# Optimization experiments

Measured on AMD Instinct MI355X. Metric: run time of the kernel, lower is better.

The kernel has to match this reference:

```python
import jax, jax.numpy as jnp
import numpy as np

N_ROI = 1024
N_CLASS = 21      # num_classes + 1
APP_DIM = 1024
D_F = 128
N_REL = 16
DIM_K = 64
DIM_G = 64


def loc2bbox(src, loc):
    # src, loc: [M,4] with (y0,x0,y1,x1) / (dy,dx,dh,dw)
    h = src[:, 2] - src[:, 0]
    w = src[:, 3] - src[:, 1]
    cy = src[:, 0] + 0.5 * h
    cx = src[:, 1] + 0.5 * w
    ncy = loc[:, 0] * h + cy
    ncx = loc[:, 1] * w + cx
    nh = jnp.exp(loc[:, 2]) * h
    nw = jnp.exp(loc[:, 3]) * w
    return jnp.stack([ncy - 0.5 * nh, ncx - 0.5 * nw,
                      ncy + 0.5 * nh, ncx + 0.5 * nw], axis=1)


def rank_embedding(n, feat_dim, wave_len=1000.0):
    rank = jnp.arange(n, dtype=jnp.float32)[:, None]
    fr = jnp.arange(feat_dim // 2, dtype=jnp.float32)
    dim_mat = 1.0 / (wave_len ** (fr / (feat_dim / 2.0)))
    mul = rank * dim_mat[None, :]
    return jnp.concatenate([jnp.sin(mul), jnp.cos(mul)], axis=-1)  # [n, feat_dim]


def positional_embedding(f_g, dim_g, wave_len=1000.0):
    # f_g: [N,4]; replicates the repo's PositionalEmbedding exactly
    x_min, y_min, x_max, y_max = jnp.split(f_g, 4, axis=1)  # [N,1] each
    cx = (x_min + x_max) * 0.5
    cy = (y_min + y_max) * 0.5
    w = (x_max - x_min) + 1.0
    h = (y_max - y_min) + 1.0
    dx = jnp.log(jnp.maximum(jnp.abs((cx - cx.T) / w), 1e-3))
    dy = jnp.log(jnp.maximum(jnp.abs((cy - cy.T) / h), 1e-3))
    dw = jnp.log(w / w.T)
    dh = jnp.log(h / h.T)
    pos = jnp.stack([dx, dy, dw, dh], axis=-1)               # [N,N,4]
    fr = jnp.arange(dim_g // 8, dtype=jnp.float32)
    dim_mat = 1.0 / (wave_len ** (fr / (dim_g / 8.0)))       # [dim_g/8]
    mul = (100.0 * pos)[..., None] * dim_mat                 # [N,N,4,dim_g/8]
    mul = mul.reshape(pos.shape[0], pos.shape[1], -1)
    return jnp.concatenate([jnp.sin(mul), jnp.cos(mul)], axis=-1)  # [N,N,dim_g]


def setup_inputs():
    key = jax.random.key(0)
    ks = jax.random.split(key, 16)
    yx = jax.random.uniform(ks[0], (N_ROI, 2), minval=0.0, maxval=500.0)
    hw = jax.random.uniform(ks[1], (N_ROI, 2), minval=16.0, maxval=128.0)
    sample_roi = jnp.concatenate([yx, yx + hw], axis=1)      # valid (y0,x0,y1,x1)
    roi_cls_loc = jax.random.normal(ks[2], (N_ROI, N_CLASS * 4)) * 0.5
    roi_score = jax.random.normal(ks[3], (N_ROI, N_CLASS))
    # force no background argmax -> nonzero() filter keeps all N (static shapes)
    roi_score = roi_score.at[:, 0].add(-10.0)
    appearance_features = jax.random.normal(ks[4], (N_ROI, APP_DIM))
    size = jnp.array([600, 800], dtype=jnp.int32)
    s = 0.02
    rank_w = jax.random.normal(ks[5], (APP_DIM, D_F)) * s
    rank_b = jnp.zeros((D_F,), jnp.float32)
    feat_w = jax.random.normal(ks[6], (APP_DIM, D_F)) * s
    feat_b = jnp.zeros((D_F,), jnp.float32)
    logit_w = jax.random.normal(ks[7], (APP_DIM, 1)) * s
    logit_b = jnp.zeros((1,), jnp.float32)
    wg_w = jax.random.normal(ks[8], (N_REL, DIM_G)) * s
    wg_b = jnp.full((N_REL,), 0.1, jnp.float32)  # keep some geo weights > 0
    wk_w = jax.random.normal(ks[9], (N_REL, D_F, DIM_K)) * s
    wk_b = jnp.zeros((N_REL, DIM_K), jnp.float32)
    wq_w = jax.random.normal(ks[10], (N_REL, D_F, DIM_K)) * s
    wq_b = jnp.zeros((N_REL, DIM_K), jnp.float32)
    wv_w = jax.random.normal(ks[11], (N_REL, D_F, DIM_K)) * s
    wv_b = jnp.zeros((N_REL, DIM_K), jnp.float32)
    return {"sample_roi": sample_roi, "roi_cls_loc": roi_cls_loc,
            "roi_score": roi_score, "appearance_features": appearance_features,
            "size": size,
            "rank_w": rank_w, "rank_b": rank_b, "feat_w": feat_w, "feat_b": feat_b,
            "logit_w": logit_w, "logit_b": logit_b,
            "wg_w": wg_w, "wg_b": wg_b, "wk_w": wk_w, "wk_b": wk_b,
            "wq_w": wq_w, "wq_b": wq_b, "wv_w": wv_w, "wv_b": wv_b}


def reference(sample_roi, roi_cls_loc, roi_score, appearance_features, size,
              rank_w, rank_b, feat_w, feat_b, logit_w, logit_b,
              wg_w, wg_b, wk_w, wk_b, wq_w, wq_b, wv_w, wv_b):
    n = sample_roi.shape[0]
    size_f = size.astype(jnp.float32)
    # loc denormalization (mean = 0)
    std = jnp.tile(jnp.array([0.1, 0.1, 0.2, 0.2], jnp.float32), N_CLASS)
    loc = (roi_cls_loc * std).reshape(-1, 4)                  # [N*21,4]
    roi_rep = jnp.broadcast_to(sample_roi[:, None, :], (n, N_CLASS, 4)).reshape(-1, 4)
    cls_bbox = loc2bbox(roi_rep, loc).reshape(n, N_CLASS, 4)
    # replicates original's clamp on class-strided slices of the [N,21,4] view
    cls_bbox = cls_bbox.at[:, 0::2].set(jnp.clip(cls_bbox[:, 0::2], 0.0, size_f[0]))
    cls_bbox = cls_bbox.at[:, 1::2].set(jnp.clip(cls_bbox[:, 1::2], 0.0, size_f[1]))
    prob_all = jax.nn.softmax(roi_score, axis=1)
    prob = jnp.max(prob_all, axis=-1)
    prob_argmax = jnp.argmax(prob_all, axis=-1)
    cls_bbox = cls_bbox[jnp.arange(n), prob_argmax]           # [N,4]
    # background filter; inputs guarantee all foreground -> static size n
    nz = jnp.nonzero(prob_argmax, size=n, fill_value=0)[0]
    prob_argmax = prob_argmax[nz]
    prob = prob[nz]
    cls_bbox = cls_bbox[nz]
    feats = appearance_features[nz]
    order = jnp.argsort(-prob)                                # descending
    sorted_prob = prob[order]
    sorted_cls_bboxes = cls_bbox[order]
    sorted_labels = prob_argmax[order]
    sorted_features = feats[order]
    nms_rank = rank_embedding(n, APP_DIM) @ rank_w + rank_b   # [N,D_F]
    emb_feat = sorted_features @ feat_w + feat_b + nms_rank   # [N,D_F]
    pos_emb = positional_embedding(sorted_cls_bboxes, DIM_G)  # [N,N,DIM_G]
    # 16 independent RelationUnits, batched as heads h
    w_g = jax.nn.relu(jnp.einsum('mng,hg->hmn', pos_emb, wg_w) + wg_b[:, None, None])
    k = jnp.einsum('nd,hdk->hnk', emb_feat, wk_w) + wk_b[:, None, :]
    q = jnp.einsum('nd,hdk->hnk', emb_feat, wq_w) + wq_b[:, None, :]
    v = jnp.einsum('nd,hdk->hnk', emb_feat, wv_w) + wv_b[:, None, :]
    # scaled_dot[m,n] = k_m . q_n (row m is 'key', softmax over n) per original
    scores = jnp.einsum('hmk,hnk->hmn', k, q) / np.sqrt(DIM_K).astype(np.float32)
    w_mn = jax.nn.softmax(jnp.log(jnp.maximum(w_g, 1e-6)) + scores, axis=-1)
    rel = jnp.einsum('hmn,hnk->hmk', w_mn, v)                 # [H,N,K]
    rel = rel.transpose(1, 0, 2).reshape(n, N_REL * DIM_K) + sorted_features
    s1 = jax.nn.sigmoid(rel @ logit_w + logit_b).reshape(-1)
    nms_scores = s1 * sorted_prob
    return nms_scores, sorted_labels - 1, sorted_cls_bboxes
```

## Files before the change

kernel.cpp:

```cpp
#include <hip/hip_runtime.h>
#include <hip/hip_bf16.h>
#include <math.h>

typedef unsigned long long u64;
typedef unsigned int u32;
typedef __hip_bfloat16 bf16;

#define N 1024
#define NCLS 21
#define APP 1024
#define DF 128
#define NH 16
#define DK 64
#define NS 4

typedef __attribute__((ext_vector_type(8))) short short8v;
typedef __attribute__((ext_vector_type(4))) float float4v;
union U4S8 { uint4 u; short8v s; };

__device__ __forceinline__ float b2f(bf16 x) { return __bfloat162float(x); }
__device__ __forceinline__ ushort f2bu(float x) { bf16 b = __float2bfloat16(x); return *(ushort*)&b; }

__global__ void k_prep(const float* __restrict__ roi, const float* __restrict__ cls_loc,
                       const float* __restrict__ score, const int* __restrict__ size,
                       float* __restrict__ prob, int* __restrict__ label,
                       float* __restrict__ bbox, u64* __restrict__ keys)
{
    int i = blockIdx.x * 256 + threadIdx.x;
    if (i >= N) return;
    float s[NCLS];
    float mx = -1e30f; int am = 0;
    for (int c = 0; c < NCLS; c++) {
        s[c] = score[i * NCLS + c];
        if (s[c] > mx) { mx = s[c]; am = c; }
    }
    float sum = 0.f;
    for (int c = 0; c < NCLS; c++) sum += expf(s[c] - mx);
    float p = 1.0f / sum;

    float y0 = roi[i*4+0], x0 = roi[i*4+1];
    float y1 = roi[i*4+2], x1 = roi[i*4+3];
    float hh = y1 - y0, ww = x1 - x0;
    float cy = y0 + 0.5f * hh, cx = x0 + 0.5f * ww;
    float l0 = cls_loc[i*84 + am*4 + 0] * 0.1f;
    float l1 = cls_loc[i*84 + am*4 + 1] * 0.1f;
    float l2 = cls_loc[i*84 + am*4 + 2] * 0.2f;
    float l3 = cls_loc[i*84 + am*4 + 3] * 0.2f;
    float ncy = l0 * hh + cy, ncx = l1 * ww + cx;
    float nh = expf(l2) * hh, nw = expf(l3) * ww;
    float b0 = ncy - 0.5f * nh, b1 = ncx - 0.5f * nw;
    float b2v = ncy + 0.5f * nh, b3 = ncx + 0.5f * nw;
    float lim = ((am & 1) == 0) ? (float)size[0] : (float)size[1];
    b0  = fminf(fmaxf(b0, 0.f), lim);
    b1  = fminf(fmaxf(b1, 0.f), lim);
    b2v = fminf(fmaxf(b2v, 0.f), lim);
    b3  = fminf(fmaxf(b3, 0.f), lim);
    prob[i] = p; label[i] = am;
    bbox[i*4+0] = b0; bbox[i*4+1] = b1; bbox[i*4+2] = b2v; bbox[i*4+3] = b3;
    keys[i] = ((u64)(0xFFFFFFFFu - __float_as_uint(p)) << 32) | (u32)i;
}

__global__ void __launch_bounds__(256) k_rank(
        const u64* __restrict__ keys, const float* __restrict__ prob,
        const int* __restrict__ label, const float* __restrict__ bbox,
        int* __restrict__ order, float* __restrict__ sprob,
        float* __restrict__ sbbox, float* __restrict__ out)
{
    __shared__ u64 sk[N];
    int t = threadIdx.x;
    int i = blockIdx.x * 256 + t;
    for (int j = t; j < N; j += 256) sk[j] = keys[j];
    __syncthreads();
    u64 my = sk[i];
    int r = 0;
    for (int j = 0; j < N; j++) r += (sk[j] < my) ? 1 : 0;
    order[r] = i;
    sprob[r] = prob[i];
    float b0 = bbox[i*4+0], b1 = bbox[i*4+1], b2 = bbox[i*4+2], b3 = bbox[i*4+3];
    sbbox[r*4+0] = b0; sbbox[r*4+1] = b1; sbbox[r*4+2] = b2; sbbox[r*4+3] = b3;
    out[N + r] = (float)(label[i] - 1);
    out[2*N + r*4 + 0] = b0;
    out[2*N + r*4 + 1] = b1;
    out[2*N + r*4 + 2] = b2;
    out[2*N + r*4 + 3] = b3;
}

__global__ void __launch_bounds__(256) k_emb3(
        const int* __restrict__ order, const float* __restrict__ app,
        const float* __restrict__ feat_w, const float* __restrict__ rank_w,
        float* __restrict__ part)
{
    __shared__ ushort sA[64][72];
    __shared__ ushort sW[128][72];
    __shared__ int sOrd[64];
    int rt = blockIdx.x, dc = blockIdx.y, ph = blockIdx.z, t = threadIdx.x;
    int r0 = rt * 64, d0 = dc * 64;
    int w = t >> 6, l = t & 63, l15 = l & 15, quad = l >> 4;
    if (t < 64) sOrd[t] = order[r0 + t];
    __syncthreads();

    const float* Wsrc = ph ? rank_w : feat_w;
    #pragma unroll
    for (int it = 0; it < 32; it++) {
        int idx = t + it * 256;
        int d = idx >> 7, c = idx & 127;
        sW[c][d] = f2bu(Wsrc[(size_t)(d0 + d) * 128 + c]);
    }
    if (ph == 0) {
        #pragma unroll
        for (int it = 0; it < 16; it++) {
            int idx = t + it * 256;
            int r = idx >> 6, d = idx & 63;
            sA[r][d] = f2bu(app[(size_t)sOrd[r] * 1024 + d0 + d]);
        }
    } else {
        #pragma unroll
        for (int it = 0; it < 16; it++) {
            int idx = t + it * 256;
            int r = idx >> 6, d = idx & 63;
            int dgl = d0 + d;
            float irow = (float)(r0 + r);
            float val;
            if (dgl < 512) val = __sinf(irow * exp2f(-(float)dgl * 0.019464422f));
            else           val = __cosf(irow * exp2f(-(float)(dgl - 512) * 0.019464422f));
            sA[r][d] = f2bu(val);
        }
    }
    __syncthreads();

    U4S8 Af0, Af1;
    Af0.u = *(uint4*)&sA[w*16 + l15][quad*8];
    Af1.u = *(uint4*)&sA[w*16 + l15][32 + quad*8];
    float4v acc[8];
    #pragma unroll
    for (int nb = 0; nb < 8; nb++) acc[nb] = (float4v){0.f, 0.f, 0.f, 0.f};
    #pragma unroll
    for (int nb = 0; nb < 8; nb++) {
        U4S8 Bf0, Bf1;
        Bf0.u = *(uint4*)&sW[nb*16 + l15][quad*8];
        Bf1.u = *(uint4*)&sW[nb*16 + l15][32 + quad*8];
        acc[nb] = __builtin_amdgcn_mfma_f32_16x16x32_bf16(Af0.s, Bf0.s, acc[nb], 0, 0, 0);
        acc[nb] = __builtin_amdgcn_mfma_f32_16x16x32_bf16(Af1.s, Bf1.s, acc[nb], 0, 0, 0);
    }
    #pragma unroll
    for (int reg = 0; reg < 4; reg++) {
        int row = r0 + w*16 + quad*4 + reg;
        #pragma unroll
        for (int nb = 0; nb < 8; nb++)
            part[(((size_t)ph * 16 + dc) * 1024 + row) * 128 + nb*16 + l15] = acc[nb][reg];
    }
}

__global__ void k_embsum(const float* __restrict__ part,
                         const float* __restrict__ feat_b, const float* __restrict__ rank_b,
                         bf16* __restrict__ embb)
{
    int gid = blockIdx.x * 256 + threadIdx.x;
    int c = gid & 127;
    float acc = feat_b[c] + rank_b[c];
    for (int dc = 0; dc < 32; dc++) acc += part[(size_t)dc * 131072 + gid];
    embb[gid] = __float2bfloat16(acc);
}

__global__ void __launch_bounds__(256) k_qkv2(
        const bf16* __restrict__ embb,
        const float* __restrict__ wq, const float* __restrict__ bq,
        const float* __restrict__ wk, const float* __restrict__ bk,
        const float* __restrict__ wv, const float* __restrict__ bv,
        bf16* __restrict__ q, bf16* __restrict__ k, bf16* __restrict__ v)
{
    __shared__ ushort sWt[64][136];
    int t = threadIdx.x;
    int rt = blockIdx.x, h = blockIdx.y, mat = blockIdx.z;
    const float* W  = (mat == 0) ? wq : (mat == 1) ? wk : wv;
    const float* Bb = (mat == 0) ? bq : (mat == 1) ? bk : bv;
    bf16* Out       = (mat == 0) ? q  : (mat == 1) ? k  : v;

    #pragma unroll
    for (int i = 0; i < 32; i++) {
        int idx = t + i * 256;
        int d = idx >> 6, kk = idx & 63;
        sWt[kk][d] = f2bu(W[((size_t)h * 128 + d) * 64 + kk]);
    }
    int w = t >> 6, l = t & 63, l15 = l & 15, quad = l >> 4;
    float biasv[4];
    #pragma unroll
    for (int nb = 0; nb < 4; nb++) biasv[nb] = Bb[h * 64 + nb*16 + l15];
    __syncthreads();

    U4S8 Bf[4][4];
    #pragma unroll
    for (int nb = 0; nb < 4; nb++)
        #pragma unroll
        for (int kc = 0; kc < 4; kc++)
            Bf[nb][kc].u = *(uint4*)&sWt[nb*16 + l15][kc*32 + quad*8];

    const uint4* A4 = (const uint4*)embb;
    int r0 = rt * 128 + w * 32;
    ushort* outu = (ushort*)Out;
    for (int mb = 0; mb < 2; mb++) {
        int arow = r0 + mb*16 + l15;
        U4S8 Af[4];
        #pragma unroll
        for (int kc = 0; kc < 4; kc++) Af[kc].u = A4[(size_t)arow * 16 + kc*4 + quad];
        float4v acc[4];
        #pragma unroll
        for (int nb = 0; nb < 4; nb++) acc[nb] = (float4v){0.f, 0.f, 0.f, 0.f};
        #pragma unroll
        for (int kc = 0; kc < 4; kc++)
            #pragma unroll
            for (int nb = 0; nb < 4; nb++)
                acc[nb] = __builtin_amdgcn_mfma_f32_16x16x32_bf16(Af[kc].s, Bf[nb][kc].s, acc[nb], 0, 0, 0);
        #pragma unroll
        for (int reg = 0; reg < 4; reg++) {
            int orow = r0 + mb*16 + quad*4 + reg;
            #pragma unroll
            for (int nb = 0; nb < 4; nb++)
                outu[((size_t)h * N + orow) * 64 + nb*16 + l15] = f2bu(acc[nb][reg] + biasv[nb]);
        }
    }
}

__global__ void __launch_bounds__(256) k_geo2(
        const float* __restrict__ sbbox, const float* __restrict__ wgw,
        const float* __restrict__ wgb, bf16* __restrict__ lw)
{
    __shared__ ushort sE[256][72];
    __shared__ uint   sOut[NH][132];
    __shared__ float  mbb[4];
    int m = blockIdx.x, nc = blockIdx.y, t = threadIdx.x;
    int w = t >> 6, l = t & 63, l15 = l & 15, quad = l >> 4;

    if (t == 0) {
        float b0 = sbbox[m*4+0], b1 = sbbox[m*4+1], b2 = sbbox[m*4+2], b3 = sbbox[m*4+3];
        mbb[0] = (b0 + b2) * 0.5f; mbb[1] = (b1 + b3) * 0.5f;
        mbb[2] = b2 - b0 + 1.0f;   mbb[3] = b3 - b1 + 1.0f;
    }
    U4S8 Bg0, Bg1;
    #pragma unroll
    for (int j = 0; j < 8; j++) {
        ((ushort*)&Bg0)[j] = f2bu(wgw[l15*64 + quad*8 + j]);
        ((ushort*)&Bg1)[j] = f2bu(wgw[l15*64 + 32 + quad*8 + j]);
    }
    float bias = wgb[l15];
    __syncthreads();

    int n = nc * 256 + t;
    float b0 = sbbox[n*4+0], b1 = sbbox[n*4+1], b2 = sbbox[n*4+2], b3 = sbbox[n*4+3];
    float cxn = (b0 + b2) * 0.5f, cyn = (b1 + b3) * 0.5f;
    float wn = b2 - b0 + 1.0f, hn = b3 - b1 + 1.0f;
    float dx = __logf(fmaxf(fabsf((mbb[0] - cxn) / mbb[2]), 1e-3f));
    float dy = __logf(fmaxf(fabsf((mbb[1] - cyn) / mbb[3]), 1e-3f));
    float dw = __logf(mbb[2] / wn);
    float dh = __logf(mbb[3] / hn);
    float pos[4] = { dx, dy, dw, dh };
    const float dmt[8] = { 1.0f, 0.42169650342f, 0.177827941f, 0.0749894209f,
                           0.0316227766f, 0.01333521432f, 0.00562341325f, 0.00237137371f };
    float args[32];
    #pragma unroll
    for (int c = 0; c < 4; c++)
        #pragma unroll
        for (int f = 0; f < 8; f++) args[c*8 + f] = 100.0f * pos[c] * dmt[f];
    uint* rowp = (uint*)&sE[t][0];
    #pragma unroll
    for (int jj = 0; jj < 16; jj++) {
        float s0 = __sinf(args[2*jj]), s1 = __sinf(args[2*jj+1]);
        rowp[jj] = (uint)f2bu(s0) | ((uint)f2bu(s1) << 16);
    }
    #pragma unroll
    for (int jj = 0; jj < 16; jj++) {
        float c0 = __cosf(args[2*jj]), c1 = __cosf(args[2*jj+1]);
        rowp[16 + jj] = (uint)f2bu(c0) | ((uint)f2bu(c1) << 16);
    }
    __syncthreads();

    #pragma unroll
    for (int mt2 = 0; mt2 < 4; mt2++) {
        int prow = w*64 + mt2*16 + l15;
        U4S8 Af0, Af1;
        Af0.u = *(uint4*)&sE[prow][quad*8];
        Af1.u = *(uint4*)&sE[prow][32 + quad*8];
        float4v c = (float4v){0.f, 0.f, 0.f, 0.f};
        c = __builtin_amdgcn_mfma_f32_16x16x32_bf16(Af0.s, Bg0.s, c, 0, 0, 0);
        c = __builtin_amdgcn_mfma_f32_16x16x32_bf16(Af1.s, Bg1.s, c, 0, 0, 0);
        float v0 = __logf(fmaxf(fmaxf(c[0] + bias, 0.f), 1e-6f));
        float v1 = __logf(fmaxf(fmaxf(c[1] + bias, 0.f), 1e-6f));
        float v2 = __logf(fmaxf(fmaxf(c[2] + bias, 0.f), 1e-6f));
        float v3 = __logf(fmaxf(fmaxf(c[3] + bias, 0.f), 1e-6f));
        int pb = (w*64 + mt2*16 + quad*4) >> 1;
        sOut[l15][pb]     = (uint)f2bu(v0) | ((uint)f2bu(v1) << 16);
        sOut[l15][pb + 1] = (uint)f2bu(v2) | ((uint)f2bu(v3) << 16);
    }
    __syncthreads();
    uint* lwu = (uint*)lw;
    #pragma unroll
    for (int it = 0; it < 8; it++) {
        int idx = t + it * 256;
        int hh = idx >> 7, col = idx & 127;
        lwu[((size_t)hh << 19) + ((size_t)m << 9) + nc*128 + col] = sOut[hh][col];
    }
}

__global__ void __launch_bounds__(256) k_attn4(
        const bf16* __restrict__ q, const bf16* __restrict__ kmat,
        const bf16* __restrict__ v, const bf16* __restrict__ lw,
        float* __restrict__ opart, float* __restrict__ mpart, float* __restrict__ zpart)
{
    __shared__ uint sQu[64][36];
    __shared__ uint sVtu[64][36];
    __shared__ uint slwu[64][36];
    __shared__ uint sPu[4][16][36];

    int t = threadIdx.x;
    int mt = blockIdx.x, h = blockIdx.y, ns = blockIdx.z;
    int m0 = mt * 64;
    int w = t >> 6, l = t & 63, l15 = l & 15, quad = l >> 4;

    U4S8 kf0, kf1;
    {
        const uint4* k4 = (const uint4*)kmat;
        size_t krow = ((size_t)h * N + m0 + w*16 + l15) * 8;
        kf0.u = k4[krow + quad];
        kf1.u = k4[krow + 4 + quad];
    }

    float4v O[4];
    float M[4], Z[4];
    #pragma unroll
    for (int i = 0; i < 4; i++) {
        O[i] = (float4v){0.f, 0.f, 0.f, 0.f};
        M[i] = -1e30f; Z[i] = 0.f;
    }

    const uint* qsrc = (const uint*)q;
    const uint* vsrc = (const uint*)v;
    const uint* lwsrc = (const uint*)lw;

    for (int tile = ns * (16/NS); tile < (ns + 1) * (16/NS); tile++) {
        int n0 = tile * 64;
        #pragma unroll
        for (int i = 0; i < 8; i++) {
            int idx = t + i * 256;
            int nj = idx >> 5, kp = idx & 31;
            sQu[nj][kp] = qsrc[((size_t)h * N + n0 + nj) * 32 + kp];
        }
        #pragma unroll
        for (int i = 0; i < 4; i++) {
            int idx = t + i * 256;
            int a = idx & 31, nh2 = idx >> 5;
            uint g0 = vsrc[((size_t)h * N + n0 + 2*nh2) * 32 + a];
            uint g1 = vsrc[((size_t)h * N + n0 + 2*nh2 + 1) * 32 + a];
            sVtu[2*a][nh2]     = (g0 & 0xFFFFu) | (g1 << 16);
            sVtu[2*a + 1][nh2] = (g0 >> 16) | (g1 & 0xFFFF0000u);
        }
        #pragma unroll
        for (int i = 0; i < 8; i++) {
            int idx = t + i * 256;
            int mi = idx >> 5, np = idx & 31;
            slwu[mi][np] = lwsrc[((size_t)h << 19) + ((size_t)(m0 + mi) << 9) + (n0 >> 1) + np];
        }
        __syncthreads();

        float4v S[4];
        #pragma unroll
        for (int nb = 0; nb < 4; nb++) {
            U4S8 bq0, bq1;
            bq0.u = *(uint4*)&sQu[nb*16 + l15][quad*4];
            bq1.u = *(uint4*)&sQu[nb*16 + l15][16 + quad*4];
            float4v zz = (float4v){0.f, 0.f, 0.f, 0.f};
            float4v p0 = __builtin_amdgcn_mfma_f32_16x16x32_bf16(kf0.s, bq0.s, zz, 0, 0, 0);
            S[nb] = __builtin_amdgcn_mfma_f32_16x16x32_bf16(kf1.s, bq1.s, p0, 0, 0, 0);
        }
        ushort* pRow[4];
        #pragma unroll
        for (int r = 0; r < 4; r++) pRow[r] = (ushort*)&sPu[w][quad*4 + r][0];
        #pragma unroll
        for (int r = 0; r < 4; r++) {
            int mi = w*16 + quad*4 + r;
            float sv[4];
            #pragma unroll
            for (int nb = 0; nb < 4; nb++) {
                int col = nb*16 + l15;
                uint lu = slwu[mi][col >> 1];
                float lv = (col & 1) ? __uint_as_float(lu & 0xFFFF0000u)
                                     : __uint_as_float(lu << 16);
                sv[nb] = S[nb][r] * 0.125f + lv;
            }
            float rm = fmaxf(fmaxf(sv[0], sv[1]), fmaxf(sv[2], sv[3]));
            #pragma unroll
            for (int off = 1; off < 16; off <<= 1)
                rm = fmaxf(rm, __shfl_xor(rm, off, 64));
            float newM = fmaxf(M[r], rm);
            float pr[4], rs = 0.f;
            #pragma unroll
            for (int nb = 0; nb < 4; nb++) {
                pr[nb] = __expf(sv[nb] - newM);
                rs += pr[nb];
            }
            #pragma unroll
            for (int off = 1; off < 16; off <<= 1)
                rs += __shfl_xor(rs, off, 64);
            float sc = __expf(M[r] - newM);
            M[r] = newM;
            Z[r] = Z[r] * sc + rs;
            #pragma unroll
            for (int kvb = 0; kvb < 4; kvb++) O[kvb][r] *= sc;
            #pragma unroll
            for (int nb = 0; nb < 4; nb++)
                pRow[r][nb*16 + l15] = f2bu(pr[nb]);
        }
        {
            U4S8 ap0, ap1;
            ap0.u = *(uint4*)&sPu[w][l15][quad*4];
            ap1.u = *(uint4*)&sPu[w][l15][16 + quad*4];
            #pragma unroll
            for (int kvb = 0; kvb < 4; kvb++) {
                U4S8 bv0, bv1;
                bv0.u = *(uint4*)&sVtu[kvb*16 + l15][quad*4];
                bv1.u = *(uint4*)&sVtu[kvb*16 + l15][16 + quad*4];
                O[kvb] = __builtin_amdgcn_mfma_f32_16x16x32_bf16(ap0.s, bv0.s, O[kvb], 0, 0, 0);
                O[kvb] = __builtin_amdgcn_mfma_f32_16x16x32_bf16(ap1.s, bv1.s, O[kvb], 0, 0, 0);
            }
        }
        __syncthreads();
    }

    #pragma unroll
    for (int r = 0; r < 4; r++) {
        int m = m0 + w*16 + quad*4 + r;
        size_t row = ((size_t)ns * NH + h) * N + m;
        #pragma unroll
        for (int kvb = 0; kvb < 4; kvb++)
            opart[row * 64 + kvb*16 + l15] = O[kvb][r];
        if (l15 == 0) { mpart[row] = M[r]; zpart[row] = Z[r]; }
    }
}

__global__ void __launch_bounds__(256) k_amerge(
        const float* __restrict__ opart, const float* __restrict__ mpart,
        const float* __restrict__ zpart, bf16* __restrict__ rel)
{
    int gid = blockIdx.x * 256 + threadIdx.x;
    int row = gid >> 4;
    int colq = gid & 15;
    float Ms[NS];
    float Mg = -1e30f;
    #pragma unroll
    for (int ns = 0; ns < NS; ns++) {
        Ms[ns] = mpart[(size_t)ns * 16384 + row];
        Mg = fmaxf(Mg, Ms[ns]);
    }
    float Zt = 0.f;
    float acc0 = 0.f, acc1 = 0.f, acc2 = 0.f, acc3 = 0.f;
    #pragma unroll
    for (int ns = 0; ns < NS; ns++) {
        float wgt = __expf(Ms[ns] - Mg);
        Zt += zpart[(size_t)ns * 16384 + row] * wgt;
        float4 o = *(const float4*)&opart[((size_t)ns * 16384 + row) * 64 + colq*4];
        acc0 += o.x * wgt; acc1 += o.y * wgt; acc2 += o.z * wgt; acc3 += o.w * wgt;
    }
    float inv = 1.0f / Zt;
    ushort* relu = (ushort*)rel;
    size_t base = (size_t)row * 64 + colq*4;
    relu[base + 0] = f2bu(acc0 * inv);
    relu[base + 1] = f2bu(acc1 * inv);
    relu[base + 2] = f2bu(acc2 * inv);
    relu[base + 3] = f2bu(acc3 * inv);
}

__global__ void k_final(const bf16* __restrict__ rel, const int* __restrict__ order,
                        const float* __restrict__ app, const float* __restrict__ lw,
                        const float* __restrict__ lb, const float* __restrict__ sprob,
                        float* __restrict__ out)
{
    __shared__ float red[2];
    int m = blockIdx.x, t = threadIdx.x;
    int o = order[m];
    float s = 0.f;
    for (int j = t; j < APP; j += 128) {
        int hh = j >> 6, kk = j & 63;
        float rv = b2f(rel[((size_t)hh * N + m) * DK + kk]) + app[o * APP + j];
        s += rv * lw[j];
    }
    #pragma unroll
    for (int off = 32; off > 0; off >>= 1) s += __shfl_down(s, off, 64);
    if ((t & 63) == 0) red[t >> 6] = s;
    __syncthreads();
    if (t == 0) {
        float tot = red[0] + red[1] + lb[0];
        float s1 = 1.0f / (1.0f + expf(-tot));
        out[m] = s1 * sprob[m];
    }
}

extern "C" void kernel_launch(void* const* d_in, const int* in_sizes, int n_in,
                              void* d_out, int out_size, void* d_ws, size_t ws_size,
                              hipStream_t stream)
{
    const float* roi      = (const float*)d_in[0];
    const float* cls_loc  = (const float*)d_in[1];
    const float* score    = (const float*)d_in[2];
    const float* app      = (const float*)d_in[3];
    const int*   size     = (const int*)d_in[4];
    const float* rank_w   = (const float*)d_in[5];
    const float* rank_b   = (const float*)d_in[6];
    const float* feat_w   = (const float*)d_in[7];
    const float* feat_b   = (const float*)d_in[8];
    const float* logit_w  = (const float*)d_in[9];
    const float* logit_b  = (const float*)d_in[10];
    const float* wg_w     = (const float*)d_in[11];
    const float* wg_b     = (const float*)d_in[12];
    const float* wk_w     = (const float*)d_in[13];
    const float* wk_b     = (const float*)d_in[14];
    const float* wq_w     = (const float*)d_in[15];
    const float* wq_b     = (const float*)d_in[16];
    const float* wv_w     = (const float*)d_in[17];
    const float* wv_b     = (const float*)d_in[18];
    float* out = (float*)d_out;

    char* ws = (char*)d_ws;
    float* prob  = (float*)(ws + 0);
    int*   label = (int*)  (ws + 4096);
    float* bbox  = (float*)(ws + 8192);
    u64*   keys  = (u64*)  (ws + 24576);
    int*   order = (int*)  (ws + 32768);
    float* sprob = (float*)(ws + 36864);
    float* sbbox = (float*)(ws + 40960);
    bf16*  embb  = (bf16*) (ws + 57344);
    bf16*  q     = (bf16*) (ws + 8970240);
    bf16*  k     = (bf16*) (ws + 11067392);
    bf16*  v     = (bf16*) (ws + 13164544);
    bf16*  rel   = (bf16*) (ws + 15261696);
    bf16*  lwbuf = (bf16*) (ws + 17358848);
    float* part  = (float*)(ws + 50913280);
    float* opart = (float*)(ws + 67690496);
    float* mpart = (float*)(ws + 84467712);
    float* zpart = (float*)(ws + 84729856);

    k_prep<<<4, 256, 0, stream>>>(roi, cls_loc, score, size, prob, label, bbox, keys);
    k_rank<<<4, 256, 0, stream>>>(keys, prob, label, bbox, order, sprob, sbbox, out);
    k_emb3<<<dim3(16, 16, 2), 256, 0, stream>>>(order, app, feat_w, rank_w, part);
    k_embsum<<<512, 256, 0, stream>>>(part, feat_b, rank_b, embb);
    k_qkv2<<<dim3(8, 16, 3), 256, 0, stream>>>(embb, wq_w, wq_b, wk_w, wk_b, wv_w, wv_b, q, k, v);
    k_geo2<<<dim3(1024, 4), 256, 0, stream>>>(sbbox, wg_w, wg_b, lwbuf);
    k_attn4<<<dim3(16, 16, NS), 256, 0, stream>>>(q, k, v, lwbuf, opart, mpart, zpart);
    k_amerge<<<1024, 256, 0, stream>>>(opart, mpart, zpart, rel);
    k_final<<<1024, 128, 0, stream>>>(rel, order, app, logit_w, logit_b, sprob, out);
}
```

Baseline: 190.5 us.

## Fuse prep/rank, merge attention split-K into final, shrink embedding partials

Merges the prep and rank kernels into one single-block kernel that computes keys in registers and ranks them in shared memory. The embedding GEMM now loops over four K-chunks per block, so it writes 8 partial slabs instead of 32 and the reduction reads less. The attention partial outputs are stored as bf16 and the merge kernel is removed, with the softmax-split combine folded into the final logit kernel. This cuts two launches and a large amount of partial-buffer traffic, at the cost of less parallelism in the embedding and prep stages and some extra bf16 rounding of partial outputs.

Result: slower. 194.9 us (+2.3%).

```diff
diff --git a/kernel.cpp b/kernel.cpp
--- a/kernel.cpp
+++ b/kernel.cpp
@@ -20,14 +20,16 @@
 
 __device__ __forceinline__ float b2f(bf16 x) { return __bfloat162float(x); }
 __device__ __forceinline__ ushort f2bu(float x) { bf16 b = __float2bfloat16(x); return *(ushort*)&b; }
-
-__global__ void k_prep(const float* __restrict__ roi, const float* __restrict__ cls_loc,
-                       const float* __restrict__ score, const int* __restrict__ size,
-                       float* __restrict__ prob, int* __restrict__ label,
-                       float* __restrict__ bbox, u64* __restrict__ keys)
-{
-    int i = blockIdx.x * 256 + threadIdx.x;
-    if (i >= N) return;
+__device__ __forceinline__ float bu2f(ushort u) { return __uint_as_float(((uint)u) << 16); }
+
+__global__ void __launch_bounds__(1024) k_prepsort(
+        const float* __restrict__ roi, const float* __restrict__ cls_loc,
+        const float* __restrict__ score, const int* __restrict__ size,
+        int* __restrict__ order, float* __restrict__ sprob,
+        float* __restrict__ sbbox, float* __restrict__ out)
+{
+    __shared__ u64 sk[N];
+    int i = threadIdx.x;
     float s[NCLS];
     float mx = -1e30f; int am = 0;
     for (int c = 0; c < NCLS; c++) {
@@ -55,37 +57,23 @@
     b1  = fminf(fmaxf(b1, 0.f), lim);
     b2v = fminf(fmaxf(b2v, 0.f), lim);
     b3  = fminf(fmaxf(b3, 0.f), lim);
-    prob[i] = p; label[i] = am;
-    bbox[i*4+0] = b0; bbox[i*4+1] = b1; bbox[i*4+2] = b2v; bbox[i*4+3] = b3;
-    keys[i] = ((u64)(0xFFFFFFFFu - __float_as_uint(p)) << 32) | (u32)i;
-}
-
-__global__ void __launch_bounds__(256) k_rank(
-        const u64* __restrict__ keys, const float* __restrict__ prob,
-        const int* __restrict__ label, const float* __restrict__ bbox,
-        int* __restrict__ order, float* __restrict__ sprob,
-        float* __restrict__ sbbox, float* __restrict__ out)
-{
-    __shared__ u64 sk[N];
-    int t = threadIdx.x;
-    int i = blockIdx.x * 256 + t;
-    for (int j = t; j < N; j += 256) sk[j] = keys[j];
-    __syncthreads();
-    u64 my = sk[i];
+
+    u64 my = ((u64)(0xFFFFFFFFu - __float_as_uint(p)) << 32) | (u32)i;
+    sk[i] = my;
+    __syncthreads();
     int r = 0;
     for (int j = 0; j < N; j++) r += (sk[j] < my) ? 1 : 0;
     order[r] = i;
-    sprob[r] = prob[i];
-    float b0 = bbox[i*4+0], b1 = bbox[i*4+1], b2 = bbox[i*4+2], b3 = bbox[i*4+3];
-    sbbox[r*4+0] = b0; sbbox[r*4+1] = b1; sbbox[r*4+2] = b2; sbbox[r*4+3] = b3;
-    out[N + r] = (float)(label[i] - 1);
+    sprob[r] = p;
+    sbbox[r*4+0] = b0; sbbox[r*4+1] = b1; sbbox[r*4+2] = b2v; sbbox[r*4+3] = b3;
+    out[N + r] = (float)(am - 1);
     out[2*N + r*4 + 0] = b0;
     out[2*N + r*4 + 1] = b1;
-    out[2*N + r*4 + 2] = b2;
+    out[2*N + r*4 + 2] = b2v;
     out[2*N + r*4 + 3] = b3;
 }
 
-__global__ void __launch_bounds__(256) k_emb3(
+__global__ void __launch_bounds__(256) k_emb4(
         const int* __restrict__ order, const float* __restrict__ app,
         const float* __restrict__ feat_w, const float* __restrict__ rank_w,
         float* __restrict__ part)
@@ -93,61 +81,65 @@
     __shared__ ushort sA[64][72];
     __shared__ ushort sW[128][72];
     __shared__ int sOrd[64];
-    int rt = blockIdx.x, dc = blockIdx.y, ph = blockIdx.z, t = threadIdx.x;
-    int r0 = rt * 64, d0 = dc * 64;
+    int rt = blockIdx.x, dg = blockIdx.y, ph = blockIdx.z, t = threadIdx.x;
+    int r0 = rt * 64;
     int w = t >> 6, l = t & 63, l15 = l & 15, quad = l >> 4;
     if (t < 64) sOrd[t] = order[r0 + t];
     __syncthreads();
 
     const float* Wsrc = ph ? rank_w : feat_w;
-    #pragma unroll
-    for (int it = 0; it < 32; it++) {
-        int idx = t + it * 256;
-        int d = idx >> 7, c = idx & 127;
-        sW[c][d] = f2bu(Wsrc[(size_t)(d0 + d) * 128 + c]);
-    }
-    if (ph == 0) {
-        #pragma unroll
-        for (int it = 0; it < 16; it++) {
+    float4v acc[8];
+    #pragma unroll
+    for (int nb = 0; nb < 8; nb++) acc[nb] = (float4v){0.f, 0.f, 0.f, 0.f};
+
+    for (int dc = dg * 4; dc < dg * 4 + 4; dc++) {
+        int d0 = dc * 64;
+        #pragma unroll
+        for (int it = 0; it < 32; it++) {
             int idx = t + it * 256;
-            int r = idx >> 6, d = idx & 63;
-            sA[r][d] = f2bu(app[(size_t)sOrd[r] * 1024 + d0 + d]);
-        }
-    } else {
-        #pragma unroll
-        for (int it = 0; it < 16; it++) {
-            int idx = t + it * 256;
-            int r = idx >> 6, d = idx & 63;
-            int dgl = d0 + d;
-            float irow = (float)(r0 + r);
-            float val;
-            if (dgl < 512) val = __sinf(irow * exp2f(-(float)dgl * 0.019464422f));
-            else           val = __cosf(irow * exp2f(-(float)(dgl - 512) * 0.019464422f));
-            sA[r][d] = f2bu(val);
-        }
-    }
-    __syncthreads();
-
-    U4S8 Af0, Af1;
-    Af0.u = *(uint4*)&sA[w*16 + l15][quad*8];
-    Af1.u = *(uint4*)&sA[w*16 + l15][32 + quad*8];
-    float4v acc[8];
-    #pragma unroll
-    for (int nb = 0; nb < 8; nb++) acc[nb] = (float4v){0.f, 0.f, 0.f, 0.f};
-    #pragma unroll
-    for (int nb = 0; nb < 8; nb++) {
-        U4S8 Bf0, Bf1;
-        Bf0.u = *(uint4*)&sW[nb*16 + l15][quad*8];
-        Bf1.u = *(uint4*)&sW[nb*16 + l15][32 + quad*8];
-        acc[nb] = __builtin_amdgcn_mfma_f32_16x16x32_bf16(Af0.s, Bf0.s, acc[nb], 0, 0, 0);
-        acc[nb] = __builtin_amdgcn_mfma_f32_16x16x32_bf16(Af1.s, Bf1.s, acc[nb], 0, 0, 0);
+            int d = idx >> 7, c = idx & 127;
+            sW[c][d] = f2bu(Wsrc[(size_t)(d0 + d) * 128 + c]);
+        }
+        if (ph == 0) {
+            #pragma unroll
+            for (int it = 0; it < 16; it++) {
+                int idx = t + it * 256;
+                int r = idx >> 6, d = idx & 63;
+                sA[r][d] = f2bu(app[(size_t)sOrd[r] * 1024 + d0 + d]);
+            }
+        } else {
+            #pragma unroll
+            for (int it = 0; it < 16; it++) {
+                int idx = t + it * 256;
+                int r = idx >> 6, d = idx & 63;
+                int dgl = d0 + d;
+                float irow = (float)(r0 + r);
+                float val;
+                if (dgl < 512) val = __sinf(irow * exp2f(-(float)dgl * 0.019464422f));
+                else           val = __cosf(irow * exp2f(-(float)(dgl - 512) * 0.019464422f));
+                sA[r][d] = f2bu(val);
+            }
+        }
+        __syncthreads();
+        U4S8 Af0, Af1;
+        Af0.u = *(uint4*)&sA[w*16 + l15][quad*8];
+        Af1.u = *(uint4*)&sA[w*16 + l15][32 + quad*8];
+        #pragma unroll
+        for (int nb = 0; nb < 8; nb++) {
+            U4S8 Bf0, Bf1;
+            Bf0.u = *(uint4*)&sW[nb*16 + l15][quad*8];
+            Bf1.u = *(uint4*)&sW[nb*16 + l15][32 + quad*8];
+            acc[nb] = __builtin_amdgcn_mfma_f32_16x16x32_bf16(Af0.s, Bf0.s, acc[nb], 0, 0, 0);
+            acc[nb] = __builtin_amdgcn_mfma_f32_16x16x32_bf16(Af1.s, Bf1.s, acc[nb], 0, 0, 0);
+        }
+        __syncthreads();
     }
     #pragma unroll
     for (int reg = 0; reg < 4; reg++) {
         int row = r0 + w*16 + quad*4 + reg;
         #pragma unroll
         for (int nb = 0; nb < 8; nb++)
-            part[(((size_t)ph * 16 + dc) * 1024 + row) * 128 + nb*16 + l15] = acc[nb][reg];
+            part[(((size_t)ph * 4 + dg) * 1024 + row) * 128 + nb*16 + l15] = acc[nb][reg];
     }
 }
 
@@ -158,7 +150,8 @@
     int gid = blockIdx.x * 256 + threadIdx.x;
     int c = gid & 127;
     float acc = feat_b[c] + rank_b[c];
-    for (int dc = 0; dc < 32; dc++) acc += part[(size_t)dc * 131072 + gid];
+    #pragma unroll
+    for (int p8 = 0; p8 < 8; p8++) acc += part[(size_t)p8 * 131072 + gid];
     embb[gid] = __float2bfloat16(acc);
 }
 
@@ -304,7 +297,7 @@
 __global__ void __launch_bounds__(256) k_attn4(
         const bf16* __restrict__ q, const bf16* __restrict__ kmat,
         const bf16* __restrict__ v, const bf16* __restrict__ lw,
-        float* __restrict__ opart, float* __restrict__ mpart, float* __restrict__ zpart)
+        bf16* __restrict__ opartb, float* __restrict__ mpart, float* __restrict__ zpart)
 {
     __shared__ uint sQu[64][36];
     __shared__ uint sVtu[64][36];
@@ -425,61 +418,58 @@
         __syncthreads();
     }
 
+    ushort* ob = (ushort*)opartb;
     #pragma unroll
     for (int r = 0; r < 4; r++) {
         int m = m0 + w*16 + quad*4 + r;
         size_t row = ((size_t)ns * NH + h) * N + m;
         #pragma unroll
         for (int kvb = 0; kvb < 4; kvb++)
-            opart[row * 64 + kvb*16 + l15] = O[kvb][r];
+            ob[row * 64 + kvb*16 + l15] = f2bu(O[kvb][r]);
         if (l15 == 0) { mpart[row] = M[r]; zpart[row] = Z[r]; }
     }
 }
 
-__global__ void __launch_bounds__(256) k_amerge(
-        const float* __restrict__ opart, const float* __restrict__ mpart,
-        const float* __restrict__ zpart, bf16* __restrict__ rel)
-{
-    int gid = blockIdx.x * 256 + threadIdx.x;
-    int row = gid >> 4;
-    int colq = gid & 15;
-    float Ms[NS];
-    float Mg = -1e30f;
-    #pragma unroll
-    for (int ns = 0; ns < NS; ns++) {
-        Ms[ns] = mpart[(size_t)ns * 16384 + row];
-        Mg = fmaxf(Mg, Ms[ns]);
-    }
-    float Zt = 0.f;
-    float acc0 = 0.f, acc1 = 0.f, acc2 = 0.f, acc3 = 0.f;
-    #pragma unroll
-    for (int ns = 0; ns < NS; ns++) {
-        float wgt = __expf(Ms[ns] - Mg);
-        Zt += zpart[(size_t)ns * 16384 + row] * wgt;
-        float4 o = *(const float4*)&opart[((size_t)ns * 16384 + row) * 64 + colq*4];
-        acc0 += o.x * wgt; acc1 += o.y * wgt; acc2 += o.z * wgt; acc3 += o.w * wgt;
-    }
-    float inv = 1.0f / Zt;
-    ushort* relu = (ushort*)rel;
-    size_t base = (size_t)row * 64 + colq*4;
-    relu[base + 0] = f2bu(acc0 * inv);
-    relu[base + 1] = f2bu(acc1 * inv);
-    relu[base + 2] = f2bu(acc2 * inv);
-    relu[base + 3] = f2bu(acc3 * inv);
-}
-
-__global__ void k_final(const bf16* __restrict__ rel, const int* __restrict__ order,
-                        const float* __restrict__ app, const float* __restrict__ lw,
-                        const float* __restrict__ lb, const float* __restrict__ sprob,
-                        float* __restrict__ out)
-{
+__global__ void __launch_bounds__(128) k_final2(
+        const bf16* __restrict__ opartb, const float* __restrict__ mpart,
+        const float* __restrict__ zpart, const int* __restrict__ order,
+        const float* __restrict__ app, const float* __restrict__ lw,
+        const float* __restrict__ lb, const float* __restrict__ sprob,
+        float* __restrict__ out)
+{
+    __shared__ float sWgt[NH][NS];
+    __shared__ float sInvZ[NH];
     __shared__ float red[2];
     int m = blockIdx.x, t = threadIdx.x;
+    if (t < NH) {
+        int h = t;
+        float Ms[NS], Mg = -1e30f;
+        #pragma unroll
+        for (int ns = 0; ns < NS; ns++) {
+            Ms[ns] = mpart[(size_t)ns * 16384 + h * 1024 + m];
+            Mg = fmaxf(Mg, Ms[ns]);
+        }
+        float Zt = 0.f;
+        #pragma unroll
+        for (int ns = 0; ns < NS; ns++) {
+            float wgt = __expf(Ms[ns] - Mg);
+            sWgt[h][ns] = wgt;
+            Zt += zpart[(size_t)ns * 16384 + h * 1024 + m] * wgt;
+        }
+        sInvZ[h] = 1.0f / Zt;
+    }
+    __syncthreads();
     int o = order[m];
+    const ushort* ob = (const ushort*)opartb;
     float s = 0.f;
     for (int j = t; j < APP; j += 128) {
         int hh = j >> 6, kk = j & 63;
-        float rv = b2f(rel[((size_t)hh * N + m) * DK + kk]) + app[o * APP + j];
+        size_t base = ((size_t)hh * 1024 + m) * 64 + kk;
+        float val = 0.f;
+        #pragma unroll
+        for (int ns = 0; ns < NS; ns++)
+            val += bu2f(ob[(size_t)ns * 1048576 + base]) * sWgt[hh][ns];
+        float rv = val * sInvZ[hh] + app[o * APP + j];
         s += rv * lw[j];
     }
     #pragma unroll
@@ -519,10 +509,6 @@
     float* out = (float*)d_out;
 
     char* ws = (char*)d_ws;
-    float* prob  = (float*)(ws + 0);
-    int*   label = (int*)  (ws + 4096);
-    float* bbox  = (float*)(ws + 8192);
-    u64*   keys  = (u64*)  (ws + 24576);
     int*   order = (int*)  (ws + 32768);
     float* sprob = (float*)(ws + 36864);
     float* sbbox = (float*)(ws + 40960);
@@ -530,20 +516,17 @@
     bf16*  q     = (bf16*) (ws + 8970240);
     bf16*  k     = (bf16*) (ws + 11067392);
     bf16*  v     = (bf16*) (ws + 13164544);
-    bf16*  rel   = (bf16*) (ws + 15261696);
     bf16*  lwbuf = (bf16*) (ws + 17358848);
     float* part  = (float*)(ws + 50913280);
-    float* opart = (float*)(ws + 67690496);
+    bf16*  opartb= (bf16*) (ws + 67690496);
     float* mpart = (float*)(ws + 84467712);
     float* zpart = (float*)(ws + 84729856);
 
-    k_prep<<<4, 256, 0, stream>>>(roi, cls_loc, score, size, prob, label, bbox, keys);
-    k_rank<<<4, 256, 0, stream>>>(keys, prob, label, bbox, order, sprob, sbbox, out);
-    k_emb3<<<dim3(16, 16, 2), 256, 0, stream>>>(order, app, feat_w, rank_w, part);
+    k_prepsort<<<1, 1024, 0, stream>>>(roi, cls_loc, score, size, order, sprob, sbbox, out);
+    k_emb4<<<dim3(16, 4, 2), 256, 0, stream>>>(order, app, feat_w, rank_w, part);
     k_embsum<<<512, 256, 0, stream>>>(part, feat_b, rank_b, embb);
     k_qkv2<<<dim3(8, 16, 3), 256, 0, stream>>>(embb, wq_w, wq_b, wk_w, wk_b, wv_w, wv_b, q, k, v);
     k_geo2<<<dim3(1024, 4), 256, 0, stream>>>(sbbox, wg_w, wg_b, lwbuf);
-    k_attn4<<<dim3(16, 16, NS), 256, 0, stream>>>(q, k, v, lwbuf, opart, mpart, zpart);
-    k_amerge<<<1024, 256, 0, stream>>>(opart, mpart, zpart, rel);
-    k_final<<<1024, 128, 0, stream>>>(rel, order, app, logit_w, logit_b, sprob, out);
-}
+    k_attn4<<<dim3(16, 16, NS), 256, 0, stream>>>(q, k, v, lwbuf, opartb, mpart, zpart);
+    k_final2<<<1024, 128, 0, stream>>>(opartb, mpart, zpart, order, app, logit_w, logit_b, sprob, out);
+}
```
